# Performance work log

Measured on AMD Instinct MI355X. Metric: run time of the kernel, lower is better.

The kernel has to match this reference:

```python
import jax, jax.numpy as jnp
import numpy as np

B, N, F_IN, F_OUT = 8, 2048, 64, 64
NEG = -9.0e15  # matches torch's -9000000000000000.0 mask value


def setup_inputs() -> dict:
    key = jax.random.key(0)
    ks = jax.random.split(key, 12)
    stdv1 = 1.0 / np.sqrt(F_IN)
    stdv2 = 1.0 / np.sqrt(2 * F_OUT)
    x = jax.random.normal(ks[0], (B, N, F_IN), dtype=jnp.float32)
    adj = jax.random.randint(ks[1], (B, N, N), 0, 2).astype(jnp.int32)
    identity = jnp.broadcast_to(jnp.eye(N, dtype=jnp.int32), (B, N, N))
    def unif(k, shape, s):
        return jax.random.uniform(k, shape, jnp.float32, -s, s)
    return {
        "x": x, "adj": adj, "identity": identity,
        "W1": unif(ks[2], (F_OUT, F_IN), stdv1), "b1": unif(ks[3], (F_OUT,), stdv1),
        "a1": unif(ks[4], (1, 2 * F_OUT), stdv2), "ab1": unif(ks[5], (1,), stdv2),
        "W2": unif(ks[6], (F_OUT, F_IN), stdv1), "b2": unif(ks[7], (F_OUT,), stdv1),
        "a2": unif(ks[8], (1, 2 * F_OUT), stdv2), "ab2": unif(ks[9], (1,), stdv2),
    }


def _gat_layer(x, mask, W, b, a, ab):
    # linear1
    h = jnp.einsum('bnf,of->bno', x, W) + b                     # [B,N,Fo]
    Fo = h.shape[-1]
    # linear2 on concat(h_i, h_j) decomposes: e_ij = relu(h_i.a1 + h_j.a2 + ab)
    s1 = h @ a[0, :Fo]                                          # [B,N]
    s2 = h @ a[0, Fo:]                                          # [B,N]
    e = jax.nn.relu(s1[:, :, None] + s2[:, None, :] + ab[0])    # [B,N,N]
    e = jnp.where(mask > 0, e, NEG)
    att = jax.nn.softmax(e, axis=2)                             # [B,N,N]
    return jnp.einsum('bnm,bmf->bnf', att, h)                   # dropout p=0 / eval


def reference(x, adj, identity, W1, b1, a1, ab1, W2, b2, a2, ab2):
    out1 = _gat_layer(x, adj, W1, b1, a1, ab1)
    out2 = _gat_layer(x, identity, W2, b2, a2, ab2)
    return out1 + out2
```

## Files before the change

### kernel.cpp

```cpp
#include <hip/hip_runtime.h>


#define DEVI __device__ __forceinline__

typedef __attribute__((ext_vector_type(8))) short short8;
typedef __attribute__((ext_vector_type(4))) float floatx4;

DEVI unsigned short f2bf(float x) {
    unsigned u = __builtin_bit_cast(unsigned, x);
    unsigned r = u + 0x7FFFu + ((u >> 16) & 1u);
    return (unsigned short)(r >> 16);
}

DEVI short8 pack8(const float* v) {
    short8 r;
#pragma unroll
    for (int i = 0; i < 8; ++i) r[i] = (short)f2bf(v[i]);
    return r;
}

DEVI unsigned cvt_pk_bf16(float lo, float hi) {
    unsigned r;
    asm("v_cvt_pk_bf16_f32 %0, %1, %2" : "=v"(r) : "v"(lo), "v"(hi));
    return r;
}

__global__ __launch_bounds__(256) void k_prep(
    const float* __restrict__ x, const float* __restrict__ W1,
    const float* __restrict__ b1, const float* __restrict__ a1,
    const float* __restrict__ ab1,
    unsigned short* __restrict__ hT1,
    float* __restrict__ t1,
    float* __restrict__ s2a)
{
    __shared__ __align__(16) unsigned short hstage[64][72];
    const int tid = threadIdx.x;
    const int w = tid >> 6, lane = tid & 63;
    const int g = lane >> 4, r15 = lane & 15;
    const int blockRow = blockIdx.x * 64;
    const int rowbase = blockRow + w * 16;

    float xa[8], xb[8];
    const float* xrow = x + (long)(rowbase + r15) * 64;
#pragma unroll
    for (int e = 0; e < 8; ++e) { xa[e] = xrow[g * 8 + e]; xb[e] = xrow[32 + g * 8 + e]; }
    short8 A0 = pack8(xa), A1 = pack8(xb);

    floatx4 acc[4];
#pragma unroll
    for (int nt = 0; nt < 4; ++nt) {
        float wa[8], wb[8];
        const float* wrow = W1 + (nt * 16 + r15) * 64;
#pragma unroll
        for (int e = 0; e < 8; ++e) { wa[e] = wrow[g * 8 + e]; wb[e] = wrow[32 + g * 8 + e]; }
        short8 B0 = pack8(wa), B1 = pack8(wb);
        floatx4 c = {0.f, 0.f, 0.f, 0.f};
        c = __builtin_amdgcn_mfma_f32_16x16x32_bf16(A0, B0, c, 0, 0, 0);
        c = __builtin_amdgcn_mfma_f32_16x16x32_bf16(A1, B1, c, 0, 0, 0);
        float bias = b1[nt * 16 + r15];
#pragma unroll
        for (int q = 0; q < 4; ++q) c[q] += bias;
        acc[nt] = c;
    }

    float a1lo[4], a1hi[4];
#pragma unroll
    for (int nt = 0; nt < 4; ++nt) {
        a1lo[nt] = a1[nt * 16 + r15];
        a1hi[nt] = a1[64 + nt * 16 + r15];
    }
    float s1q[4], s2q[4];
#pragma unroll
    for (int q = 0; q < 4; ++q) {
        float s1 = 0.f, s2 = 0.f;
#pragma unroll
        for (int nt = 0; nt < 4; ++nt) { s1 += acc[nt][q] * a1lo[nt]; s2 += acc[nt][q] * a1hi[nt]; }
#pragma unroll
        for (int m = 1; m < 16; m <<= 1) { s1 += __shfl_xor(s1, m); s2 += __shfl_xor(s2, m); }
        s1q[q] = s1; s2q[q] = s2;
    }
    if (r15 == 0) {
        float abv = ab1[0];
#pragma unroll
        for (int q = 0; q < 4; ++q) {
            t1[rowbase + 4 * g + q] = s1q[q] + abv;
            s2a[rowbase + 4 * g + q] = s2q[q];
        }
    }

#pragma unroll
    for (int nt = 0; nt < 4; ++nt)
#pragma unroll
        for (int q = 0; q < 4; ++q)
            hstage[nt * 16 + r15][w * 16 + 4 * g + q] = f2bf(acc[nt][q]);
    __syncthreads();
    {
        const int o = tid >> 2, seg = (tid & 3) * 16;
        const int bb = blockRow >> 11;
        const int ib = blockRow & 2047;
        unsigned short* dst = hT1 + ((long)(bb * 64 + o) * 2048) + ib + seg;
        uint4 v0 = *(const uint4*)&hstage[o][seg];
        uint4 v1 = *(const uint4*)&hstage[o][seg + 8];
        *(uint4*)dst = v0;
        *(uint4*)(dst + 8) = v1;
    }
}

__global__ __launch_bounds__(512) void k_attn(
    const float* __restrict__ x, const int* __restrict__ adj,
    const float* __restrict__ W2, const float* __restrict__ b2,
    const unsigned short* __restrict__ hT1,
    const float* __restrict__ t1, const float* __restrict__ s2a,
    float* __restrict__ out)
{
    __shared__ __align__(16) unsigned short plds[8][16][72];
    __shared__ __align__(16) float accbuf[4][16][64];
    __shared__ __align__(16) float h2buf[4][16][64];
    __shared__ float ldenom[2][4][16];

    const int tid = threadIdx.x;
    const int w = tid >> 6, lane = tid & 63;
    const int t = w >> 2, wrow = w & 3;
    const int g = lane >> 4, r15 = lane & 15;
    const int bb = blockIdx.x >> 5;
    const int i0 = (blockIdx.x & 31) * 64;
    const int rowbase = i0 + wrow * 16;
    const int jbase = t * 16;

    float tr4[4];
#pragma unroll
    for (int rr = 0; rr < 4; ++rr) tr4[rr] = t1[bb * 2048 + rowbase + rr * 4 + g];
    float lpart[4];
#pragma unroll
    for (int rr = 0; rr < 4; ++rr) lpart[rr] = 0.f;
    floatx4 acc[4];
#pragma unroll
    for (int nt = 0; nt < 4; ++nt) acc[nt] = (floatx4){0.f, 0.f, 0.f, 0.f};

    const int4* adjq = (const int4*)(adj + (long)(bb * 2048 + rowbase + g) * 2048) + r15;
    const float4* s2q = (const float4*)(s2a + (long)bb * 2048) + r15;
    const unsigned short* hbase = hT1 + (long)(bb * 64 + r15) * 2048 + g * 8;

    int4 adjA[4], adjB[4];
    float4 A_s2, B_s2;
    short8 b0A[4], b1A[4], b0B[4], b1B[4];

#define LOADSET(S, c) do {                                                     \
        const int jc_ = jbase + (c);                                           \
        S##_s2 = s2q[jc_ * 16];                                                \
        _Pragma("unroll")                                                      \
        for (int rr_ = 0; rr_ < 4; ++rr_) adj##S[rr_] = adjq[rr_ * 2048 + jc_ * 16]; \
        _Pragma("unroll")                                                      \
        for (int nt_ = 0; nt_ < 4; ++nt_) {                                    \
            b0##S[nt_] = *(const short8*)(hbase + nt_ * 32768 + jc_ * 64);     \
            b1##S[nt_] = *(const short8*)(hbase + nt_ * 32768 + jc_ * 64 + 32);\
        }                                                                      \
    } while (0)

#define COMPUTE(S) do {                                                        \
        _Pragma("unroll")                                                      \
        for (int rr_ = 0; rr_ < 4; ++rr_) {                                    \
            float z0 = fmaxf(tr4[rr_] + S##_s2.x, 0.f);                        \
            float z1 = fmaxf(tr4[rr_] + S##_s2.y, 0.f);                        \
            float z2 = fmaxf(tr4[rr_] + S##_s2.z, 0.f);                        \
            float z3 = fmaxf(tr4[rr_] + S##_s2.w, 0.f);                        \
            float p0 = adj##S[rr_].x > 0 ? __expf(z0) : 0.f;                   \
            float p1 = adj##S[rr_].y > 0 ? __expf(z1) : 0.f;                   \
            float p2 = adj##S[rr_].z > 0 ? __expf(z2) : 0.f;                   \
            float p3 = adj##S[rr_].w > 0 ? __expf(z3) : 0.f;                   \
            lpart[rr_] += (p0 + p1) + (p2 + p3);                               \
            uint2 u;                                                           \
            u.x = cvt_pk_bf16(p0, p1);                                         \
            u.y = cvt_pk_bf16(p2, p3);                                         \
            *(uint2*)&plds[w][rr_ * 4 + g][r15 * 4] = u;                       \
        }                                                                      \
        short8 a0 = *(const short8*)&plds[w][r15][g * 8];                      \
        short8 a1 = *(const short8*)&plds[w][r15][32 + g * 8];                 \
        _Pragma("unroll")                                                      \
        for (int nt_ = 0; nt_ < 4; ++nt_) {                                    \
            acc[nt_] = __builtin_amdgcn_mfma_f32_16x16x32_bf16(a0, b0##S[nt_], acc[nt_], 0, 0, 0); \
            acc[nt_] = __builtin_amdgcn_mfma_f32_16x16x32_bf16(a1, b1##S[nt_], acc[nt_], 0, 0, 0); \
        }                                                                      \
    } while (0)

    LOADSET(A, 0);
    LOADSET(B, 1);
#pragma unroll 2
    for (int ith = 0; ith < 8; ++ith) {
        COMPUTE(A);
        if (ith < 7) LOADSET(A, 2 * ith + 2);
        COMPUTE(B);
        if (ith < 7) LOADSET(B, 2 * ith + 3);
    }
#undef LOADSET
#undef COMPUTE

#pragma unroll
    for (int rr = 0; rr < 4; ++rr) {
        float v = lpart[rr];
#pragma unroll
        for (int m = 1; m < 16; m <<= 1) v += __shfl_xor(v, m);
        if (r15 == 0) ldenom[t][wrow][rr * 4 + g] = v;
    }

    if (t == 1) {
#pragma unroll
        for (int nt = 0; nt < 4; ++nt)
#pragma unroll
            for (int q = 0; q < 4; ++q)
                accbuf[wrow][4 * g + q][nt * 16 + r15] = acc[nt][q];
        float xa[8], xb[8];
        const float* xrow = x + ((long)(bb * 2048 + rowbase + r15)) * 64;
#pragma unroll
        for (int e = 0; e < 8; ++e) { xa[e] = xrow[g * 8 + e]; xb[e] = xrow[32 + g * 8 + e]; }
        short8 A0 = pack8(xa), A1 = pack8(xb);
#pragma unroll
        for (int nt = 0; nt < 4; ++nt) {
            float wa[8], wb[8];
            const float* wrow2 = W2 + (nt * 16 + r15) * 64;
#pragma unroll
            for (int e = 0; e < 8; ++e) { wa[e] = wrow2[g * 8 + e]; wb[e] = wrow2[32 + g * 8 + e]; }
            short8 B0 = pack8(wa), B1 = pack8(wb);
            floatx4 c = {0.f, 0.f, 0.f, 0.f};
            c = __builtin_amdgcn_mfma_f32_16x16x32_bf16(A0, B0, c, 0, 0, 0);
            c = __builtin_amdgcn_mfma_f32_16x16x32_bf16(A1, B1, c, 0, 0, 0);
            float bias = b2[nt * 16 + r15];
#pragma unroll
            for (int q = 0; q < 4; ++q)
                h2buf[wrow][4 * g + q][nt * 16 + r15] = c[q] + bias;
        }
    }
    __syncthreads();

    if (t == 0) {
        float linv[4];
#pragma unroll
        for (int q = 0; q < 4; ++q)
            linv[q] = 1.0f / (ldenom[0][wrow][4 * g + q] + ldenom[1][wrow][4 * g + q]);
#pragma unroll
        for (int nt = 0; nt < 4; ++nt)
#pragma unroll
            for (int q = 0; q < 4; ++q) {
                float total = acc[nt][q] + accbuf[wrow][4 * g + q][nt * 16 + r15];
                float val = total * linv[q] + h2buf[wrow][4 * g + q][nt * 16 + r15];
                out[((long)(bb * 2048 + rowbase + 4 * g + q)) * 64 + nt * 16 + r15] = val;
            }
    }
}

extern "C" void kernel_launch(void* const* d_in, const int* in_sizes, int n_in,
                              void* d_out, int out_size, void* d_ws, size_t ws_size,
                              hipStream_t stream) {
    const float* x   = (const float*)d_in[0];
    const int*   adj = (const int*)d_in[1];
    const float* W1  = (const float*)d_in[3];
    const float* b1  = (const float*)d_in[4];
    const float* a1  = (const float*)d_in[5];
    const float* ab1 = (const float*)d_in[6];
    const float* W2  = (const float*)d_in[7];
    const float* b2  = (const float*)d_in[8];

    unsigned short* hT1 = (unsigned short*)d_ws;
    float* t1  = (float*)((char*)d_ws + (size_t)8 * 64 * 2048 * 2);
    float* s2a = t1 + 8 * 2048;

    k_prep<<<256, 256, 0, stream>>>(x, W1, b1, a1, ab1, hT1, t1, s2a);
    k_attn<<<256, 512, 0, stream>>>(x, adj, W2, b2, hT1, t1, s2a, (float*)d_out);
}
```

Baseline: 49.30 us.

## Stage hT tiles in shared LDS per team and compute denominator via MFMA

Each 4-warp team now cooperatively loads the bf16 hT1 tile for a 64-column chunk into a double-buffered LDS array, and all warps read their B operands from there. Previously each warp fetched them separately from global memory. The adjacency loads are pipelined three chunks ahead. The per-row softmax denominator now comes from an extra MFMA against a ones vector, replacing the scalar partial sums and shuffle reductions. The cost is a block-wide barrier every step, more LDS use, and a denominator summed from bf16-rounded probabilities.

```diff
diff --git a/kernel.cpp b/kernel.cpp
--- a/kernel.cpp
+++ b/kernel.cpp
@@ -23,6 +23,13 @@
     unsigned r;
     asm("v_cvt_pk_bf16_f32 %0, %1, %2" : "=v"(r) : "v"(lo), "v"(hi));
     return r;
+}
+
+DEVI void team_sync() {
+    __builtin_amdgcn_sched_barrier(0);
+    asm volatile("s_waitcnt lgkmcnt(0)" ::: "memory");
+    __builtin_amdgcn_s_barrier();
+    __builtin_amdgcn_sched_barrier(0);
 }
 
 __global__ __launch_bounds__(256) void k_prep(
@@ -113,10 +120,11 @@
     const float* __restrict__ t1, const float* __restrict__ s2a,
     float* __restrict__ out)
 {
+    __shared__ __align__(16) unsigned short hl[2][2][64][72];
     __shared__ __align__(16) unsigned short plds[8][16][72];
     __shared__ __align__(16) float accbuf[4][16][64];
     __shared__ __align__(16) float h2buf[4][16][64];
-    __shared__ float ldenom[2][4][16];
+    __shared__ float denbuf[4][16];
 
     const int tid = threadIdx.x;
     const int w = tid >> 6, lane = tid & 63;
@@ -130,45 +138,58 @@
     float tr4[4];
 #pragma unroll
     for (int rr = 0; rr < 4; ++rr) tr4[rr] = t1[bb * 2048 + rowbase + rr * 4 + g];
-    float lpart[4];
-#pragma unroll
-    for (int rr = 0; rr < 4; ++rr) lpart[rr] = 0.f;
+
     floatx4 acc[4];
 #pragma unroll
     for (int nt = 0; nt < 4; ++nt) acc[nt] = (floatx4){0.f, 0.f, 0.f, 0.f};
+    floatx4 acc5 = {0.f, 0.f, 0.f, 0.f};
+
+    short8 ones;
+#pragma unroll
+    for (int i = 0; i < 8; ++i) ones[i] = (short)0x3F80;
 
     const int4* adjq = (const int4*)(adj + (long)(bb * 2048 + rowbase + g) * 2048) + r15;
-    const float4* s2q = (const float4*)(s2a + (long)bb * 2048) + r15;
-    const unsigned short* hbase = hT1 + (long)(bb * 64 + r15) * 2048 + g * 8;
-
-    int4 adjA[4], adjB[4];
-    float4 A_s2, B_s2;
-    short8 b0A[4], b1A[4], b0B[4], b1B[4];
-
-#define LOADSET(S, c) do {                                                     \
+    const float4* s2q4 = (const float4*)(s2a + (long)bb * 2048) + r15;
+
+    const int ttid = tid & 255;
+    const int so = ttid >> 2, sseg = (ttid & 3) * 16;
+    const unsigned short* hTsrc = hT1 + (long)(bb * 64 + so) * 2048 + sseg;
+    unsigned short* hldst[2] = { &hl[t][0][so][sseg], &hl[t][1][so][sseg] };
+
+    int4 adjR[4][4];
+    float4 s2R[4];
+    uint4 hrg[2][2];
+
+#define LOAD_ADJ(slot, c) do {                                                 \
         const int jc_ = jbase + (c);                                           \
-        S##_s2 = s2q[jc_ * 16];                                                \
+        s2R[slot] = s2q4[jc_ * 16];                                            \
         _Pragma("unroll")                                                      \
-        for (int rr_ = 0; rr_ < 4; ++rr_) adj##S[rr_] = adjq[rr_ * 2048 + jc_ * 16]; \
-        _Pragma("unroll")                                                      \
-        for (int nt_ = 0; nt_ < 4; ++nt_) {                                    \
-            b0##S[nt_] = *(const short8*)(hbase + nt_ * 32768 + jc_ * 64);     \
-            b1##S[nt_] = *(const short8*)(hbase + nt_ * 32768 + jc_ * 64 + 32);\
-        }                                                                      \
-    } while (0)
-
-#define COMPUTE(S) do {                                                        \
+        for (int rr_ = 0; rr_ < 4; ++rr_)                                      \
+            adjR[slot][rr_] = adjq[rr_ * 2048 + jc_ * 16];                     \
+    } while (0)
+
+#define LOAD_HT(par, c) do {                                                   \
+        const unsigned short* src_ = hTsrc + (jbase + (c)) * 64;               \
+        hrg[par][0] = *(const uint4*)src_;                                     \
+        hrg[par][1] = *(const uint4*)(src_ + 8);                               \
+    } while (0)
+
+#define STORE_HT(par) do {                                                     \
+        *(uint4*)hldst[par] = hrg[par][0];                                     \
+        *(uint4*)(hldst[par] + 8) = hrg[par][1];                               \
+    } while (0)
+
+#define COMPUTE(C, slot, buf) do {                                             \
         _Pragma("unroll")                                                      \
         for (int rr_ = 0; rr_ < 4; ++rr_) {                                    \
-            float z0 = fmaxf(tr4[rr_] + S##_s2.x, 0.f);                        \
-            float z1 = fmaxf(tr4[rr_] + S##_s2.y, 0.f);                        \
-            float z2 = fmaxf(tr4[rr_] + S##_s2.z, 0.f);                        \
-            float z3 = fmaxf(tr4[rr_] + S##_s2.w, 0.f);                        \
-            float p0 = adj##S[rr_].x > 0 ? __expf(z0) : 0.f;                   \
-            float p1 = adj##S[rr_].y > 0 ? __expf(z1) : 0.f;                   \
-            float p2 = adj##S[rr_].z > 0 ? __expf(z2) : 0.f;                   \
-            float p3 = adj##S[rr_].w > 0 ? __expf(z3) : 0.f;                   \
-            lpart[rr_] += (p0 + p1) + (p2 + p3);                               \
+            float z0 = fmaxf(tr4[rr_] + s2R[slot].x, 0.f);                     \
+            float z1 = fmaxf(tr4[rr_] + s2R[slot].y, 0.f);                     \
+            float z2 = fmaxf(tr4[rr_] + s2R[slot].z, 0.f);                     \
+            float z3 = fmaxf(tr4[rr_] + s2R[slot].w, 0.f);                     \
+            float p0 = adjR[slot][rr_].x > 0 ? __expf(z0) : 0.f;               \
+            float p1 = adjR[slot][rr_].y > 0 ? __expf(z1) : 0.f;               \
+            float p2 = adjR[slot][rr_].z > 0 ? __expf(z2) : 0.f;               \
+            float p3 = adjR[slot][rr_].w > 0 ? __expf(z3) : 0.f;               \
             uint2 u;                                                           \
             u.x = cvt_pk_bf16(p0, p1);                                         \
             u.y = cvt_pk_bf16(p2, p3);                                         \
@@ -178,30 +199,41 @@
         short8 a1 = *(const short8*)&plds[w][r15][32 + g * 8];                 \
         _Pragma("unroll")                                                      \
         for (int nt_ = 0; nt_ < 4; ++nt_) {                                    \
-            acc[nt_] = __builtin_amdgcn_mfma_f32_16x16x32_bf16(a0, b0##S[nt_], acc[nt_], 0, 0, 0); \
-            acc[nt_] = __builtin_amdgcn_mfma_f32_16x16x32_bf16(a1, b1##S[nt_], acc[nt_], 0, 0, 0); \
+            short8 b0 = *(const short8*)&hl[t][buf][nt_ * 16 + r15][g * 8];    \
+            short8 b1 = *(const short8*)&hl[t][buf][nt_ * 16 + r15][32 + g * 8]; \
+            acc[nt_] = __builtin_amdgcn_mfma_f32_16x16x32_bf16(a0, b0, acc[nt_], 0, 0, 0); \
+            acc[nt_] = __builtin_amdgcn_mfma_f32_16x16x32_bf16(a1, b1, acc[nt_], 0, 0, 0); \
         }                                                                      \
-    } while (0)
-
-    LOADSET(A, 0);
-    LOADSET(B, 1);
-#pragma unroll 2
-    for (int ith = 0; ith < 8; ++ith) {
-        COMPUTE(A);
-        if (ith < 7) LOADSET(A, 2 * ith + 2);
-        COMPUTE(B);
-        if (ith < 7) LOADSET(B, 2 * ith + 3);
-    }
-#undef LOADSET
+        acc5 = __builtin_amdgcn_mfma_f32_16x16x32_bf16(a0, ones, acc5, 0, 0, 0); \
+        acc5 = __builtin_amdgcn_mfma_f32_16x16x32_bf16(a1, ones, acc5, 0, 0, 0); \
+    } while (0)
+
+#define STEP(C) do {                                                           \
+        if ((C) <= 13) LOAD_HT((C) & 1, (C) + 2);                              \
+        if ((C) <= 12) LOAD_ADJ(((C) + 3) & 3, (C) + 3);                       \
+        if ((C) <= 14) STORE_HT(((C) + 1) & 1);                                \
+        COMPUTE((C), (C) & 3, (C) & 1);                                        \
+        team_sync();                                                           \
+    } while (0)
+
+    LOAD_ADJ(0, 0);
+    LOAD_ADJ(1, 1);
+    LOAD_ADJ(2, 2);
+    LOAD_HT(0, 0);
+    STORE_HT(0);
+    LOAD_HT(1, 1);
+    team_sync();
+
+    STEP(0);  STEP(1);  STEP(2);  STEP(3);
+    STEP(4);  STEP(5);  STEP(6);  STEP(7);
+    STEP(8);  STEP(9);  STEP(10); STEP(11);
+    STEP(12); STEP(13); STEP(14); STEP(15);
+
+#undef STEP
 #undef COMPUTE
-
-#pragma unroll
-    for (int rr = 0; rr < 4; ++rr) {
-        float v = lpart[rr];
-#pragma unroll
-        for (int m = 1; m < 16; m <<= 1) v += __shfl_xor(v, m);
-        if (r15 == 0) ldenom[t][wrow][rr * 4 + g] = v;
-    }
+#undef STORE_HT
+#undef LOAD_HT
+#undef LOAD_ADJ
 
     if (t == 1) {
 #pragma unroll
@@ -209,6 +241,10 @@
 #pragma unroll
             for (int q = 0; q < 4; ++q)
                 accbuf[wrow][4 * g + q][nt * 16 + r15] = acc[nt][q];
+        if (r15 == 0) {
+#pragma unroll
+            for (int q = 0; q < 4; ++q) denbuf[wrow][4 * g + q] = acc5[q];
+        }
         float xa[8], xb[8];
         const float* xrow = x + ((long)(bb * 2048 + rowbase + r15)) * 64;
 #pragma unroll
@@ -236,7 +272,7 @@
         float linv[4];
 #pragma unroll
         for (int q = 0; q < 4; ++q)
-            linv[q] = 1.0f / (ldenom[0][wrow][4 * g + q] + ldenom[1][wrow][4 * g + q]);
+            linv[q] = 1.0f / (acc5[q] + denbuf[wrow][4 * g + q]);
 #pragma unroll
         for (int nt = 0; nt < 4; ++nt)
 #pragma unroll
```

Measured after the change: 40.01 us. -18.8%, faster.

## Restructure attention kernel to full-row waves with LDS-staged hT and MFMA row sums

Applied to the files above, without the earlier changes.

The attention kernel shrinks from 8 to 4 waves per block. Each wave now walks all 2048 columns for its 16 rows, which removes the two-way column split and its LDS reduction and synchronisation. hT tiles are staged through a per-wave, double-buffered, XOR-swizzled LDS region, and adjacency is prefetched three chunks ahead in registers. The softmax denominator is computed with an extra MFMA against a vector of ones, and the second GAT layer's linear output is fused straight into the epilogue. The cost is that every wave loads the same hT data separately, and fewer resident waves per CU may weaken latency hiding for the bandwidth-heavy adjacency stream.

```diff
diff --git a/kernel.cpp b/kernel.cpp
--- a/kernel.cpp
+++ b/kernel.cpp
@@ -106,145 +106,147 @@
     }
 }
 
-__global__ __launch_bounds__(512) void k_attn(
+__global__ __launch_bounds__(256, 1) void k_attn(
     const float* __restrict__ x, const int* __restrict__ adj,
     const float* __restrict__ W2, const float* __restrict__ b2,
     const unsigned short* __restrict__ hT1,
     const float* __restrict__ t1, const float* __restrict__ s2a,
     float* __restrict__ out)
 {
-    __shared__ __align__(16) unsigned short plds[8][16][72];
-    __shared__ __align__(16) float accbuf[4][16][64];
-    __shared__ __align__(16) float h2buf[4][16][64];
-    __shared__ float ldenom[2][4][16];
+    __shared__ __align__(16) unsigned short hl[4][8192];
+    __shared__ __align__(16) unsigned short plds[4][16][72];
 
     const int tid = threadIdx.x;
     const int w = tid >> 6, lane = tid & 63;
-    const int t = w >> 2, wrow = w & 3;
     const int g = lane >> 4, r15 = lane & 15;
-    const int bb = blockIdx.x >> 5;
-    const int i0 = (blockIdx.x & 31) * 64;
-    const int rowbase = i0 + wrow * 16;
-    const int jbase = t * 16;
+    const int bb = blockIdx.x & 7;
+    const int it = blockIdx.x >> 3;
+    const int rowbase = it * 64 + w * 16;
+
+    const int fr8 = lane >> 3;
+    const int fsl = (lane & 7) ^ (fr8 & 7);
+    const int bs0 = g ^ (r15 & 7);
+    const int bs1 = (4 + g) ^ (r15 & 7);
+
+    unsigned short* hlw = &hl[4][0] - 8192 * (4 - w);
+    unsigned short* pw = &plds[w][0][0];
 
     float tr4[4];
 #pragma unroll
     for (int rr = 0; rr < 4; ++rr) tr4[rr] = t1[bb * 2048 + rowbase + rr * 4 + g];
-    float lpart[4];
-#pragma unroll
-    for (int rr = 0; rr < 4; ++rr) lpart[rr] = 0.f;
+
     floatx4 acc[4];
 #pragma unroll
     for (int nt = 0; nt < 4; ++nt) acc[nt] = (floatx4){0.f, 0.f, 0.f, 0.f};
+    floatx4 acc5 = {0.f, 0.f, 0.f, 0.f};
+
+    short8 ones;
+#pragma unroll
+    for (int i = 0; i < 8; ++i) ones[i] = (short)0x3F80;
 
     const int4* adjq = (const int4*)(adj + (long)(bb * 2048 + rowbase + g) * 2048) + r15;
-    const float4* s2q = (const float4*)(s2a + (long)bb * 2048) + r15;
-    const unsigned short* hbase = hT1 + (long)(bb * 64 + r15) * 2048 + g * 8;
-
-    int4 adjA[4], adjB[4];
-    float4 A_s2, B_s2;
-    short8 b0A[4], b1A[4], b0B[4], b1B[4];
-
-#define LOADSET(S, c) do {                                                     \
-        const int jc_ = jbase + (c);                                           \
-        S##_s2 = s2q[jc_ * 16];                                                \
-        _Pragma("unroll")                                                      \
-        for (int rr_ = 0; rr_ < 4; ++rr_) adj##S[rr_] = adjq[rr_ * 2048 + jc_ * 16]; \
-        _Pragma("unroll")                                                      \
-        for (int nt_ = 0; nt_ < 4; ++nt_) {                                    \
-            b0##S[nt_] = *(const short8*)(hbase + nt_ * 32768 + jc_ * 64);     \
-            b1##S[nt_] = *(const short8*)(hbase + nt_ * 32768 + jc_ * 64 + 32);\
-        }                                                                      \
-    } while (0)
-
-#define COMPUTE(S) do {                                                        \
+    const float4* s2q4 = (const float4*)(s2a + (long)bb * 2048) + r15;
+    const unsigned short* hTln = hT1 + (long)(bb * 64 + fr8) * 2048 + (lane & 7) * 8;
+
+    int4 adjR[4][4];
+    float4 s2R[4];
+    uint4 hrg[2][8];
+
+#define ADJ(c) do {                                                            \
+        s2R[(c) & 3] = s2q4[(c) * 16];                                         \
+        _Pragma("unroll")                                                      \
+        for (int rr_ = 0; rr_ < 4; ++rr_)                                      \
+            adjR[(c) & 3][rr_] = adjq[rr_ * 2048 + (c) * 16];                  \
+    } while (0)
+
+#define HTLOAD(c) do {                                                         \
+        const unsigned short* s_ = hTln + (c) * 64;                            \
+        _Pragma("unroll")                                                      \
+        for (int k_ = 0; k_ < 8; ++k_)                                         \
+            hrg[(c) & 1][k_] = *(const uint4*)(s_ + (long)k_ * 16384);         \
+    } while (0)
+
+#define HTSTORE(c) do {                                                        \
+        _Pragma("unroll")                                                      \
+        for (int k_ = 0; k_ < 8; ++k_)                                         \
+            *(uint4*)&hlw[((c) & 1) * 4096 + (k_ * 8 + fr8) * 64 + fsl * 8]    \
+                = hrg[(c) & 1][k_];                                            \
+    } while (0)
+
+#define COMPUTE(C) do {                                                        \
+        const float4 s2v_ = s2R[(C) & 3];                                      \
         _Pragma("unroll")                                                      \
         for (int rr_ = 0; rr_ < 4; ++rr_) {                                    \
-            float z0 = fmaxf(tr4[rr_] + S##_s2.x, 0.f);                        \
-            float z1 = fmaxf(tr4[rr_] + S##_s2.y, 0.f);                        \
-            float z2 = fmaxf(tr4[rr_] + S##_s2.z, 0.f);                        \
-            float z3 = fmaxf(tr4[rr_] + S##_s2.w, 0.f);                        \
-            float p0 = adj##S[rr_].x > 0 ? __expf(z0) : 0.f;                   \
-            float p1 = adj##S[rr_].y > 0 ? __expf(z1) : 0.f;                   \
-            float p2 = adj##S[rr_].z > 0 ? __expf(z2) : 0.f;                   \
-            float p3 = adj##S[rr_].w > 0 ? __expf(z3) : 0.f;                   \
-            lpart[rr_] += (p0 + p1) + (p2 + p3);                               \
+            float z0 = fmaxf(tr4[rr_] + s2v_.x, 0.f);                          \
+            float z1 = fmaxf(tr4[rr_] + s2v_.y, 0.f);                          \
+            float z2 = fmaxf(tr4[rr_] + s2v_.z, 0.f);                          \
+            float z3 = fmaxf(tr4[rr_] + s2v_.w, 0.f);                          \
+            float p0 = adjR[(C) & 3][rr_].x > 0 ? __expf(z0) : 0.f;            \
+            float p1 = adjR[(C) & 3][rr_].y > 0 ? __expf(z1) : 0.f;            \
+            float p2 = adjR[(C) & 3][rr_].z > 0 ? __expf(z2) : 0.f;            \
+            float p3 = adjR[(C) & 3][rr_].w > 0 ? __expf(z3) : 0.f;            \
             uint2 u;                                                           \
             u.x = cvt_pk_bf16(p0, p1);                                         \
             u.y = cvt_pk_bf16(p2, p3);                                         \
-            *(uint2*)&plds[w][rr_ * 4 + g][r15 * 4] = u;                       \
+            *(uint2*)&pw[(rr_ * 4 + g) * 72 + r15 * 4] = u;                    \
         }                                                                      \
-        short8 a0 = *(const short8*)&plds[w][r15][g * 8];                      \
-        short8 a1 = *(const short8*)&plds[w][r15][32 + g * 8];                 \
+        short8 a0 = *(const short8*)&pw[r15 * 72 + g * 8];                     \
+        short8 a1 = *(const short8*)&pw[r15 * 72 + 32 + g * 8];                \
+        const int bufo_ = ((C) & 1) * 4096;                                    \
         _Pragma("unroll")                                                      \
         for (int nt_ = 0; nt_ < 4; ++nt_) {                                    \
-            acc[nt_] = __builtin_amdgcn_mfma_f32_16x16x32_bf16(a0, b0##S[nt_], acc[nt_], 0, 0, 0); \
-            acc[nt_] = __builtin_amdgcn_mfma_f32_16x16x32_bf16(a1, b1##S[nt_], acc[nt_], 0, 0, 0); \
+            short8 b0 = *(const short8*)&hlw[bufo_ + (nt_ * 16 + r15) * 64 + bs0 * 8]; \
+            short8 b1 = *(const short8*)&hlw[bufo_ + (nt_ * 16 + r15) * 64 + bs1 * 8]; \
+            acc[nt_] = __builtin_amdgcn_mfma_f32_16x16x32_bf16(a0, b0, acc[nt_], 0, 0, 0); \
+            acc[nt_] = __builtin_amdgcn_mfma_f32_16x16x32_bf16(a1, b1, acc[nt_], 0, 0, 0); \
         }                                                                      \
-    } while (0)
-
-    LOADSET(A, 0);
-    LOADSET(B, 1);
-#pragma unroll 2
-    for (int ith = 0; ith < 8; ++ith) {
-        COMPUTE(A);
-        if (ith < 7) LOADSET(A, 2 * ith + 2);
-        COMPUTE(B);
-        if (ith < 7) LOADSET(B, 2 * ith + 3);
-    }
-#undef LOADSET
+        acc5 = __builtin_amdgcn_mfma_f32_16x16x32_bf16(a0, ones, acc5, 0, 0, 0); \
+        acc5 = __builtin_amdgcn_mfma_f32_16x16x32_bf16(a1, ones, acc5, 0, 0, 0); \
+    } while (0)
+
+    ADJ(0); ADJ(1); ADJ(2);
+    HTLOAD(0);
+    HTSTORE(0);
+    HTLOAD(1);
+
+#pragma unroll
+    for (int C = 0; C < 32; ++C) {
+        if (C + 2 <= 31) HTLOAD(C + 2);
+        if (C + 3 <= 31) ADJ(C + 3);
+        if (C + 1 <= 31) HTSTORE(C + 1);
+        COMPUTE(C);
+    }
+
 #undef COMPUTE
-
-#pragma unroll
-    for (int rr = 0; rr < 4; ++rr) {
-        float v = lpart[rr];
-#pragma unroll
-        for (int m = 1; m < 16; m <<= 1) v += __shfl_xor(v, m);
-        if (r15 == 0) ldenom[t][wrow][rr * 4 + g] = v;
-    }
-
-    if (t == 1) {
-#pragma unroll
-        for (int nt = 0; nt < 4; ++nt)
-#pragma unroll
-            for (int q = 0; q < 4; ++q)
-                accbuf[wrow][4 * g + q][nt * 16 + r15] = acc[nt][q];
-        float xa[8], xb[8];
-        const float* xrow = x + ((long)(bb * 2048 + rowbase + r15)) * 64;
-#pragma unroll
-        for (int e = 0; e < 8; ++e) { xa[e] = xrow[g * 8 + e]; xb[e] = xrow[32 + g * 8 + e]; }
-        short8 A0 = pack8(xa), A1 = pack8(xb);
-#pragma unroll
-        for (int nt = 0; nt < 4; ++nt) {
-            float wa[8], wb[8];
-            const float* wrow2 = W2 + (nt * 16 + r15) * 64;
-#pragma unroll
-            for (int e = 0; e < 8; ++e) { wa[e] = wrow2[g * 8 + e]; wb[e] = wrow2[32 + g * 8 + e]; }
-            short8 B0 = pack8(wa), B1 = pack8(wb);
-            floatx4 c = {0.f, 0.f, 0.f, 0.f};
-            c = __builtin_amdgcn_mfma_f32_16x16x32_bf16(A0, B0, c, 0, 0, 0);
-            c = __builtin_amdgcn_mfma_f32_16x16x32_bf16(A1, B1, c, 0, 0, 0);
-            float bias = b2[nt * 16 + r15];
-#pragma unroll
-            for (int q = 0; q < 4; ++q)
-                h2buf[wrow][4 * g + q][nt * 16 + r15] = c[q] + bias;
+#undef HTSTORE
+#undef HTLOAD
+#undef ADJ
+
+    float linv[4];
+#pragma unroll
+    for (int q = 0; q < 4; ++q) linv[q] = 1.0f / acc5[q];
+
+    float xa[8], xb[8];
+    const float* xrow = x + ((long)(bb * 2048 + rowbase + r15)) * 64;
+#pragma unroll
+    for (int e = 0; e < 8; ++e) { xa[e] = xrow[g * 8 + e]; xb[e] = xrow[32 + g * 8 + e]; }
+    short8 A0 = pack8(xa), A1 = pack8(xb);
+#pragma unroll
+    for (int nt = 0; nt < 4; ++nt) {
+        float wa[8], wb[8];
+        const float* wrow2 = W2 + (nt * 16 + r15) * 64;
+#pragma unroll
+        for (int e = 0; e < 8; ++e) { wa[e] = wrow2[g * 8 + e]; wb[e] = wrow2[32 + g * 8 + e]; }
+        short8 B0 = pack8(wa), B1 = pack8(wb);
+        floatx4 c = {0.f, 0.f, 0.f, 0.f};
+        c = __builtin_amdgcn_mfma_f32_16x16x32_bf16(A0, B0, c, 0, 0, 0);
+        c = __builtin_amdgcn_mfma_f32_16x16x32_bf16(A1, B1, c, 0, 0, 0);
+        float bias = b2[nt * 16 + r15];
+#pragma unroll
+        for (int q = 0; q < 4; ++q) {
+            float val = acc[nt][q] * linv[q] + c[q] + bias;
+            out[((long)(bb * 2048 + rowbase + 4 * g + q)) * 64 + nt * 16 + r15] = val;
         }
-    }
-    __syncthreads();
-
-    if (t == 0) {
-        float linv[4];
-#pragma unroll
-        for (int q = 0; q < 4; ++q)
-            linv[q] = 1.0f / (ldenom[0][wrow][4 * g + q] + ldenom[1][wrow][4 * g + q]);
-#pragma unroll
-        for (int nt = 0; nt < 4; ++nt)
-#pragma unroll
-            for (int q = 0; q < 4; ++q) {
-                float total = acc[nt][q] + accbuf[wrow][4 * g + q][nt * 16 + r15];
-                float val = total * linv[q] + h2buf[wrow][4 * g + q][nt * 16 + r15];
-                out[((long)(bb * 2048 + rowbase + 4 * g + q)) * 64 + nt * 16 + r15] = val;
-            }
     }
 }
 
@@ -265,5 +267,5 @@
     float* s2a = t1 + 8 * 2048;
 
     k_prep<<<256, 256, 0, stream>>>(x, W1, b1, a1, ab1, hT1, t1, s2a);
-    k_attn<<<256, 512, 0, stream>>>(x, adj, W2, b2, hT1, t1, s2a, (float*)d_out);
-}
+    k_attn<<<256, 256, 0, stream>>>(x, adj, W2, b2, hT1, t1, s2a, (float*)d_out);
+}
```

Result: faster. 41.91 us (-15.0%).
